# Optimization experiments

Measured on AMD Instinct MI355X. Metric: run time of the kernel, lower is better.

Reference implementation:

```python
import jax, jax.numpy as jnp
import numpy as np

N_ATOMS = 8192
N_SUBSYSTEMS = 64
CUTOFF = 5.0


def setup_inputs() -> dict:
    key = jax.random.key(0)
    k1, k2 = jax.random.split(key)
    positions = jax.random.normal(k1, (N_ATOMS, 3), dtype=jnp.float32)
    atomic_subsystem_indices = jnp.sort(
        jax.random.randint(k2, (N_ATOMS,), 0, N_SUBSYSTEMS)
    ).astype(jnp.int64)
    return {"positions": positions, "atomic_subsystem_indices": atomic_subsystem_indices}


def reference(positions, atomic_subsystem_indices):
    """JIT-compatible PairList forward.

    The torch original builds dynamic-size pair lists via nonzero(); here we use
    the static upper-triangular candidate set (all i<j pairs) plus a validity
    mask (same subsystem AND distance < cutoff). Invalid pair indices are -1 and
    invalid r_ij / d_ij entries are zeroed.

    Returns (pair_indices [2,P] int, d_ij [P,1], r_ij [P,3], valid_mask [P] bool).
    """
    n = positions.shape[0]
    i, j = jnp.triu_indices(n, k=1)          # P = n*(n-1)//2 candidate pairs
    pair_indices = jnp.stack([i, j])          # (2, P)

    # displacement: selected_positions[1] - selected_positions[0]
    r_ij = positions[j] - positions[i]        # (P, 3)
    d_ij = jnp.linalg.norm(r_ij, axis=-1, keepdims=True)  # (P, 1)

    same_sys = atomic_subsystem_indices[i] == atomic_subsystem_indices[j]
    valid = same_sys & (d_ij[:, 0] < CUTOFF)  # (P,)

    pair_out = jnp.where(valid[None, :], pair_indices, -1)
    m = valid[:, None].astype(positions.dtype)
    return pair_out, d_ij * m, r_ij * m, valid
```

## Files before the change

kernel.cpp:

```cpp
#include <hip/hip_runtime.h>
#include <cmath>


__global__ __launch_bounds__(256) void pairlist_kernel(
    const float* __restrict__ pos, const int* __restrict__ sub,
    float* __restrict__ out, int n, long long P) {
  long long g  = (long long)blockIdx.x * blockDim.x + threadIdx.x;
  long long p0 = g * 4;
  if (p0 >= P) return;

  const int shift = (sub[n - 1] == 0) ? 1 : 0;

  double t = 2.0 * (double)n - 1.0;
  double disc = t * t - 8.0 * (double)p0;
  int i = (int)((t - sqrt(disc)) * 0.5);
  if (i < 0) i = 0;
  if (i > n - 2) i = n - 2;
  auto T = [n](long long ii) { return ii * (2LL * n - ii - 1) / 2; };
  while (T(i + 1) <= p0) ++i;
  while (i > 0 && T(i) > p0) --i;
  int j = (int)((long long)i + 1 + (p0 - T(i)));

  int   si  = sub[i << shift];
  float pix = pos[3 * i], piy = pos[3 * i + 1], piz = pos[3 * i + 2];

  float fi[4], fj[4], fd[4], fv[4], fr[12];

#pragma unroll
  for (int k = 0; k < 4; ++k) {
    long long p = p0 + k;
    float vi = -1.0f, vj = -1.0f, vd = 0.0f, vv = 0.0f;
    float rx = 0.0f, ry = 0.0f, rz = 0.0f;
    if (p < P) {
      int sj = sub[j << shift];
      if (sj == si) {
        float dx = pos[3 * j]     - pix;
        float dy = pos[3 * j + 1] - piy;
        float dz = pos[3 * j + 2] - piz;
        float dd = sqrtf(dx * dx + dy * dy + dz * dz);
        if (dd < 5.0f) {
          vi = (float)i; vj = (float)j;
          vd = dd; vv = 1.0f;
          rx = dx; ry = dy; rz = dz;
        }
      }
      ++j;
      if (j >= n) {
        ++i;
        j = i + 1;
        if (i < n - 1) {
          si = sub[i << shift];
          pix = pos[3 * i]; piy = pos[3 * i + 1]; piz = pos[3 * i + 2];
        }
      }
    }
    fi[k] = vi; fj[k] = vj; fd[k] = vd; fv[k] = vv;
    fr[3 * k] = rx; fr[3 * k + 1] = ry; fr[3 * k + 2] = rz;
  }

  float* oi  = out;
  float* oj  = out + P;
  float* od  = out + 2 * P;
  float* orr = out + 3 * P;
  float* ov  = out + 6 * P;

  if (p0 + 4 <= P) {
    *reinterpret_cast<float4*>(oi + p0) = make_float4(fi[0], fi[1], fi[2], fi[3]);
    *reinterpret_cast<float4*>(oj + p0) = make_float4(fj[0], fj[1], fj[2], fj[3]);
    *reinterpret_cast<float4*>(od + p0) = make_float4(fd[0], fd[1], fd[2], fd[3]);
    *reinterpret_cast<float4*>(ov + p0) = make_float4(fv[0], fv[1], fv[2], fv[3]);
    float4* rb = reinterpret_cast<float4*>(orr + 3 * p0);
    rb[0] = make_float4(fr[0], fr[1], fr[2],  fr[3]);
    rb[1] = make_float4(fr[4], fr[5], fr[6],  fr[7]);
    rb[2] = make_float4(fr[8], fr[9], fr[10], fr[11]);
  } else {
    for (int k = 0; k < 4 && p0 + k < P; ++k) {
      long long p = p0 + k;
      oi[p] = fi[k]; oj[p] = fj[k]; od[p] = fd[k]; ov[p] = fv[k];
      orr[3 * p] = fr[3 * k]; orr[3 * p + 1] = fr[3 * k + 1]; orr[3 * p + 2] = fr[3 * k + 2];
    }
  }
}

extern "C" void kernel_launch(void* const* d_in, const int* in_sizes, int n_in,
                              void* d_out, int out_size, void* d_ws, size_t ws_size,
                              hipStream_t stream) {
  const float* pos = (const float*)d_in[0];
  const int*   sub = (const int*)d_in[1];
  float* out = (float*)d_out;

  long long P = (long long)out_size / 7;
  int n = (int)((1.0 + sqrt(1.0 + 8.0 * (double)P)) * 0.5 + 0.5);
  if ((long long)n * (n - 1) / 2 != P) {
    n = in_sizes[0] / 3;
    P = (long long)n * (n - 1) / 2;
  }

  long long threads = (P + 3) / 4;
  int blocks = (int)((threads + 255) / 256);
  hipLaunchKernelGGL(pairlist_kernel, dim3(blocks), dim3(256), 0, stream,
                     pos, sub, out, n, P);
}
```

Measured before the change: 171.3 us.

## Launch one block row per atom and binary-search the same-subsystem span

Replaces the flat pair-index decomposition, which solved a quadratic per thread to recover (i,j), with a 2D grid where blockIdx.y is the row i. Each block binary-searches the sorted subsystem array to find how many j share i's subsystem. Threads past that span write constant -1/0 vectors without loading positions or subsystem ids. Rows with unaligned starting offsets use scalar stores at the edges. The kernel is bound by output writes, so the gain may be limited, and many rows launch mostly idle blocks.

```diff
diff --git a/kernel.cpp b/kernel.cpp
--- a/kernel.cpp
+++ b/kernel.cpp
@@ -2,61 +2,24 @@
 #include <cmath>
 
 
-__global__ __launch_bounds__(256) void pairlist_kernel(
+__global__ __launch_bounds__(256) void pairlist_rows(
     const float* __restrict__ pos, const int* __restrict__ sub,
     float* __restrict__ out, int n, long long P) {
-  long long g  = (long long)blockIdx.x * blockDim.x + threadIdx.x;
-  long long p0 = g * 4;
-  if (p0 >= P) return;
+  const int i = blockIdx.y;
+  const int L = n - 1 - i;
+  const long long Ti = (long long)i * (2LL * n - i - 1) / 2;
+  const int a = (int)(Ti & 3);
+  const int local0 = (int)(blockIdx.x * 1024 + threadIdx.x * 4) - a;
+  if (local0 >= L) return;
 
   const int shift = (sub[n - 1] == 0) ? 1 : 0;
-
-  double t = 2.0 * (double)n - 1.0;
-  double disc = t * t - 8.0 * (double)p0;
-  int i = (int)((t - sqrt(disc)) * 0.5);
-  if (i < 0) i = 0;
-  if (i > n - 2) i = n - 2;
-  auto T = [n](long long ii) { return ii * (2LL * n - ii - 1) / 2; };
-  while (T(i + 1) <= p0) ++i;
-  while (i > 0 && T(i) > p0) --i;
-  int j = (int)((long long)i + 1 + (p0 - T(i)));
-
-  int   si  = sub[i << shift];
-  float pix = pos[3 * i], piy = pos[3 * i + 1], piz = pos[3 * i + 2];
-
-  float fi[4], fj[4], fd[4], fv[4], fr[12];
-
-#pragma unroll
-  for (int k = 0; k < 4; ++k) {
-    long long p = p0 + k;
-    float vi = -1.0f, vj = -1.0f, vd = 0.0f, vv = 0.0f;
-    float rx = 0.0f, ry = 0.0f, rz = 0.0f;
-    if (p < P) {
-      int sj = sub[j << shift];
-      if (sj == si) {
-        float dx = pos[3 * j]     - pix;
-        float dy = pos[3 * j + 1] - piy;
-        float dz = pos[3 * j + 2] - piz;
-        float dd = sqrtf(dx * dx + dy * dy + dz * dz);
-        if (dd < 5.0f) {
-          vi = (float)i; vj = (float)j;
-          vd = dd; vv = 1.0f;
-          rx = dx; ry = dy; rz = dz;
-        }
-      }
-      ++j;
-      if (j >= n) {
-        ++i;
-        j = i + 1;
-        if (i < n - 1) {
-          si = sub[i << shift];
-          pix = pos[3 * i]; piy = pos[3 * i + 1]; piz = pos[3 * i + 2];
-        }
-      }
-    }
-    fi[k] = vi; fj[k] = vj; fd[k] = vd; fv[k] = vv;
-    fr[3 * k] = rx; fr[3 * k + 1] = ry; fr[3 * k + 2] = rz;
+  const int s = sub[i << shift];
+  int lo = i + 1, hi = n;
+  while (lo < hi) {
+    int mid = (lo + hi) >> 1;
+    if (sub[mid << shift] > s) hi = mid; else lo = mid + 1;
   }
+  const int vLen = lo - (i + 1);
 
   float* oi  = out;
   float* oj  = out + P;
@@ -64,7 +27,44 @@
   float* orr = out + 3 * P;
   float* ov  = out + 6 * P;
 
-  if (p0 + 4 <= P) {
+  const long long p0 = Ti + local0;
+
+  if (local0 >= vLen && local0 >= 0 && local0 + 4 <= L) {
+    const float4 NEG = make_float4(-1.f, -1.f, -1.f, -1.f);
+    const float4 ZER = make_float4(0.f, 0.f, 0.f, 0.f);
+    *reinterpret_cast<float4*>(oi + p0) = NEG;
+    *reinterpret_cast<float4*>(oj + p0) = NEG;
+    *reinterpret_cast<float4*>(od + p0) = ZER;
+    *reinterpret_cast<float4*>(ov + p0) = ZER;
+    float4* rb = reinterpret_cast<float4*>(orr + 3 * p0);
+    rb[0] = ZER; rb[1] = ZER; rb[2] = ZER;
+    return;
+  }
+
+  const float pix = pos[3 * i], piy = pos[3 * i + 1], piz = pos[3 * i + 2];
+  float fi[4], fj[4], fd[4], fv[4], fr[12];
+
+#pragma unroll
+  for (int k = 0; k < 4; ++k) {
+    const int local = local0 + k;
+    float vi = -1.f, vj = -1.f, vd = 0.f, vv = 0.f;
+    float rx = 0.f, ry = 0.f, rz = 0.f;
+    if (local >= 0 && local < vLen) {
+      const int j = i + 1 + local;
+      const float dx = pos[3 * j]     - pix;
+      const float dy = pos[3 * j + 1] - piy;
+      const float dz = pos[3 * j + 2] - piz;
+      const float dd = sqrtf(dx * dx + dy * dy + dz * dz);
+      if (dd < 5.f) {
+        vi = (float)i; vj = (float)j; vd = dd; vv = 1.f;
+        rx = dx; ry = dy; rz = dz;
+      }
+    }
+    fi[k] = vi; fj[k] = vj; fd[k] = vd; fv[k] = vv;
+    fr[3 * k] = rx; fr[3 * k + 1] = ry; fr[3 * k + 2] = rz;
+  }
+
+  if (local0 >= 0 && local0 + 4 <= L) {
     *reinterpret_cast<float4*>(oi + p0) = make_float4(fi[0], fi[1], fi[2], fi[3]);
     *reinterpret_cast<float4*>(oj + p0) = make_float4(fj[0], fj[1], fj[2], fj[3]);
     *reinterpret_cast<float4*>(od + p0) = make_float4(fd[0], fd[1], fd[2], fd[3]);
@@ -74,10 +74,13 @@
     rb[1] = make_float4(fr[4], fr[5], fr[6],  fr[7]);
     rb[2] = make_float4(fr[8], fr[9], fr[10], fr[11]);
   } else {
-    for (int k = 0; k < 4 && p0 + k < P; ++k) {
-      long long p = p0 + k;
+    for (int k = 0; k < 4; ++k) {
+      const int local = local0 + k;
+      if (local < 0 || local >= L) continue;
+      const long long p = Ti + local;
       oi[p] = fi[k]; oj[p] = fj[k]; od[p] = fd[k]; ov[p] = fv[k];
-      orr[3 * p] = fr[3 * k]; orr[3 * p + 1] = fr[3 * k + 1]; orr[3 * p + 2] = fr[3 * k + 2];
+      orr[3 * p] = fr[3 * k]; orr[3 * p + 1] = fr[3 * k + 1];
+      orr[3 * p + 2] = fr[3 * k + 2];
     }
   }
 }
@@ -96,8 +99,7 @@
     P = (long long)n * (n - 1) / 2;
   }
 
-  long long threads = (P + 3) / 4;
-  int blocks = (int)((threads + 255) / 256);
-  hipLaunchKernelGGL(pairlist_kernel, dim3(blocks), dim3(256), 0, stream,
+  int NT = (int)((n + 1025) / 1024);
+  hipLaunchKernelGGL(pairlist_rows, dim3(NT, n - 1), dim3(256), 0, stream,
                      pos, sub, out, n, P);
 }
```

Result: slower. 248.3 us (+45.0%).
